# Performance work log

Measured on AMD Instinct MI355X. Metric: run time of the kernel, lower is better.

## Reference

```python
import jax, jax.numpy as jnp
import numpy as np

B, N, C, H = 1, 128, 128, 8
D = C // H
SCALE = D ** -0.5


def layer_norm(x, w, b, eps=1e-5):
    m = jnp.mean(x, axis=-1, keepdims=True)
    v = jnp.var(x, axis=-1, keepdims=True)
    return (x - m) * jax.lax.rsqrt(v + eps) * w + b


def setup_inputs() -> dict:
    key = jax.random.key(0)
    ks = jax.random.split(key, 8)
    s = 0.02
    return {
        "e": jax.random.normal(ks[0], (B, N, N, C), jnp.float32),
        "mask": jnp.zeros((B, N, N, 1), jnp.float32),
        "ln_w": jnp.ones((C,), jnp.float32),
        "ln_b": jnp.zeros((C,), jnp.float32),
        "w_qkv_in": jax.random.normal(ks[1], (C, 3 * C), jnp.float32) * s,
        "b_qkv_in": jnp.zeros((3 * C,), jnp.float32),
        "w_eg_in": jax.random.normal(ks[2], (C, 2 * H), jnp.float32) * s,
        "b_eg_in": jnp.zeros((2 * H,), jnp.float32),
        "w_qkv_out": jax.random.normal(ks[3], (C, 3 * C), jnp.float32) * s,
        "b_qkv_out": jnp.zeros((3 * C,), jnp.float32),
        "w_eg_out": jax.random.normal(ks[4], (C, 2 * H), jnp.float32) * s,
        "b_eg_out": jnp.zeros((2 * H,), jnp.float32),
        "w_o": jax.random.normal(ks[5], (2 * C, C), jnp.float32) * s,
        "b_o": jnp.zeros((C,), jnp.float32),
    }


def reference(e, mask, ln_w, ln_b, w_qkv_in, b_qkv_in, w_eg_in, b_eg_in,
              w_qkv_out, b_qkv_out, w_eg_out, b_eg_out, w_o, b_o):
    b, n = e.shape[0], e.shape[1]
    e_ln = layer_norm(e, ln_w, ln_b)

    # ---- incoming-edge stream ----
    qkv = e_ln @ w_qkv_in + b_qkv_in                      # [b,n,n,3C]
    Q, K, V = jnp.split(qkv, 3, axis=-1)
    Q = Q.reshape(b, n, n, D, H) * SCALE                  # bijdh
    K = K.reshape(b, n, n, D, H)
    V = V.reshape(b, n, n, D, H)
    eg = e_ln @ w_eg_in + b_eg_in                         # [b,n,n,2H]
    E_in = eg[..., :H][:, :, None, :, :]                  # [b,i,1,k,h]
    G_in = eg[..., H:][:, :, None, :, :]
    H_in = jnp.einsum('bijdh,bjkdh->bijkh', Q, K) + E_in
    mask_in = mask[:, :, None, :, :]                      # [b,i,1,k,1]
    gates_in = jax.nn.sigmoid(G_in + mask_in)
    A_in = jax.nn.softmax(H_in + mask_in, axis=3) * gates_in
    Va_in = jnp.einsum('bijkh,bjkdh->bijdh', A_in, V)

    # ---- outgoing-edge stream ----
    qkv = e_ln @ w_qkv_out + b_qkv_out
    Q, K, V = jnp.split(qkv, 3, axis=-1)
    Q = Q.reshape(b, n, n, D, H) * SCALE
    K = K.reshape(b, n, n, D, H)
    V = V.reshape(b, n, n, D, H)
    eg = e_ln @ w_eg_out + b_eg_out
    E_out = eg[..., :H][:, :, :, None, :]                 # [b,k,i,1,h]
    G_out = eg[..., H:][:, :, :, None, :]
    H_out = jnp.einsum('bijdh,bkjdh->bkijh', Q, K) + E_out
    mask_out = mask[:, :, :, None, :]                     # [b,k,i,1,1]
    gates_out = jax.nn.sigmoid(G_out + mask_out)
    A_out = jax.nn.softmax(H_out + mask_out, axis=1) * gates_out
    Va_out = jnp.einsum('bkijh,bkjdh->bijdh', A_out, V)

    Va = jnp.concatenate([Va_in, Va_out], axis=-1).reshape(b, n, n, 2 * C)
    return Va @ w_o + b_o
```

## Files before the change

kernel.cpp:

```cpp
#include <hip/hip_runtime.h>
#include <hip/hip_bf16.h>


#define NPOS 16384
#define CDIM 128

typedef __attribute__((ext_vector_type(8))) short bf16x8;
typedef __attribute__((ext_vector_type(8))) unsigned short u16x8;
typedef __attribute__((ext_vector_type(4))) float f32x4;

#define MFMA16(a, b, c) __builtin_amdgcn_mfma_f32_16x16x32_bf16((a), (b), (c), 0, 0, 0)

#define GLL16(gp, lp) __builtin_amdgcn_global_load_lds( \
    (const __attribute__((address_space(1))) void*)(gp), \
    (__attribute__((address_space(3))) void*)(lp), 16, 0, 0)

static __device__ __forceinline__ unsigned short f2bf(float x) {
    union { float f; unsigned int u; } v; v.f = x;
    unsigned int u = v.u;
    unsigned int r = u + 0x7FFFu + ((u >> 16) & 1u);
    return (unsigned short)(r >> 16);
}
static __device__ __forceinline__ float bf2f(unsigned short h) {
    union { float f; unsigned int u; } v; v.u = ((unsigned int)h) << 16; return v.f;
}

__global__ __launch_bounds__(256) void prep_kernel(
    const float* __restrict__ e, const float* __restrict__ lnw,
    const float* __restrict__ lnb, unsigned short* __restrict__ e_hl,
    const float* __restrict__ wq1, const float* __restrict__ we1,
    unsigned short* __restrict__ B1t,
    const float* __restrict__ wq2, const float* __restrict__ we2,
    unsigned short* __restrict__ B2t,
    const float* __restrict__ wo, unsigned short* __restrict__ B3t)
{
    const int t = threadIdx.x;
    const int bx = blockIdx.x;
    if (bx < 4096) {
        const int lane = t & 63;
        const int row = bx * 4 + (t >> 6);
        float2 x = *(const float2*)(e + (size_t)row * CDIM + lane * 2);
        float s = x.x + x.y, s2 = x.x * x.x + x.y * x.y;
        #pragma unroll
        for (int off = 1; off < 64; off <<= 1) {
            s  += __shfl_xor(s,  off, 64);
            s2 += __shfl_xor(s2, off, 64);
        }
        float m = s * (1.f / 128.f);
        float v = s2 * (1.f / 128.f) - m * m;
        float sc = rsqrtf(v + 1e-5f);
        float2 wv = *(const float2*)(lnw + lane * 2);
        float2 bv = *(const float2*)(lnb + lane * 2);
        float y0 = (x.x - m) * sc * wv.x + bv.x;
        float y1 = (x.y - m) * sc * wv.y + bv.y;
        unsigned short h0 = f2bf(y0), h1 = f2bf(y1);
        ushort2 hi = {h0, h1};
        ushort2 lo = {f2bf(y0 - bf2f(h0)), f2bf(y1 - bf2f(h1))};
        *(ushort2*)(e_hl + (size_t)row * 256 + lane * 2)       = hi;
        *(ushort2*)(e_hl + (size_t)row * 256 + 128 + lane * 2) = lo;
    } else if (bx < 4544) {
        int pb = bx - 4096;
        const float* wq; const float* we; unsigned short* Bt;
        if (pb < 224) { wq = wq1; we = we1; Bt = B1t; }
        else          { pb -= 224; wq = wq2; we = we2; Bt = B2t; }
        const int idx = pb * 256 + t;
        const int n = idx >> 7, k = idx & 127;
        float v = 0.f;
        if (n < 384) v = wq[(size_t)k * 384 + n];
        else if (n < 400) v = we[(size_t)k * 16 + (n - 384)];
        unsigned short hi = f2bf(v);
        Bt[idx] = hi;
        Bt[448 * 128 + idx] = f2bf(v - bf2f(hi));
    } else {
        const int idx = (bx - 4544) * 256 + t;
        const int n = idx >> 8, kp = idx & 255;
        const int d = kp & 15, pl = kp >> 4;
        const int k = d * 16 + pl;
        float v = wo[(size_t)k * 128 + n];
        unsigned short hi = f2bf(v);
        B3t[idx] = hi;
        B3t[128 * 256 + idx] = f2bf(v - bf2f(hi));
    }
}

__global__ __launch_bounds__(256) void gemm_qkv_kernel(
    const unsigned short* __restrict__ e_hl,
    const unsigned short* __restrict__ B1t, const unsigned short* __restrict__ B2t,
    const float* __restrict__ bq_i, const float* __restrict__ be_i,
    const float* __restrict__ bq_o, const float* __restrict__ be_o,
    const float* __restrict__ mask,
    unsigned short* __restrict__ QT, unsigned short* __restrict__ KT,
    unsigned short* __restrict__ VT,
    unsigned short* __restrict__ Etab, unsigned short* __restrict__ Gtab)
{
    __shared__ __align__(16) unsigned char smem[24576];
    unsigned short* Alds = (unsigned short*)smem;
    unsigned short* Blds = (unsigned short*)(smem + 16384);

    const int t = threadIdx.x;
    const int wave = t >> 6, lane = t & 63;
    const int m = lane & 15, q = lane >> 4;
    const int c = blockIdx.x;
    const int bx = ((c & 31) << 2) | (c >> 5);
    const int W0blk = bx * 128;
    const int by = blockIdx.y;
    const int N0 = by * 64;
    const int br = blockIdx.z;
    const unsigned short* Bt = br ? B2t : B1t;
    const float* bias_qkv = br ? bq_o : bq_i;
    const float* bias_eg  = br ? be_o : be_i;

    f32x4 acc[2][4];
    #pragma unroll
    for (int a = 0; a < 2; ++a)
        #pragma unroll
        for (int cc = 0; cc < 4; ++cc) acc[a][cc] = (f32x4){0.f, 0.f, 0.f, 0.f};

    for (int kc = 0; kc < 4; ++kc) {
        #pragma unroll
        for (int ii = 0; ii < 6; ++ii) {
            const int id = wave + ii * 4;
            if (id < 16) {
                const int hl = id >> 3, s = id & 7;
                const int qq = s >> 1, rbase = (s & 1) * 64;
                const unsigned short* g = e_hl
                    + (size_t)(W0blk + rbase + lane) * 256 + hl * 128 + kc * 32 + qq * 8;
                unsigned short* l = Alds + hl * 4096 + qq * 1024 + rbase * 8;
                GLL16(g, l);
            } else {
                const int id2 = id - 16;
                const int hl = id2 >> 2, qq = id2 & 3;
                const unsigned short* g = Bt + (size_t)(N0 + lane) * 128
                    + hl * (448 * 128) + kc * 32 + qq * 8;
                unsigned short* l = Blds + hl * 2048 + qq * 512;
                GLL16(g, l);
            }
        }
        __syncthreads();

        bf16x8 aH[2], aL[2], bH[4], bL[4];
        #pragma unroll
        for (int ms = 0; ms < 2; ++ms) {
            const int row = wave * 32 + ms * 16 + m;
            aH[ms] = *(const bf16x8*)(Alds + 0    + q * 1024 + row * 8);
            aL[ms] = *(const bf16x8*)(Alds + 4096 + q * 1024 + row * 8);
        }
        #pragma unroll
        for (int ns = 0; ns < 4; ++ns) {
            bH[ns] = *(const bf16x8*)(Blds + 0    + q * 512 + (ns * 16 + m) * 8);
            bL[ns] = *(const bf16x8*)(Blds + 2048 + q * 512 + (ns * 16 + m) * 8);
        }
        #pragma unroll
        for (int ns = 0; ns < 4; ++ns) {
            acc[0][ns] = MFMA16(aH[0], bH[ns], acc[0][ns]);
            acc[1][ns] = MFMA16(aH[1], bH[ns], acc[1][ns]);
        }
        #pragma unroll
        for (int ns = 0; ns < 4; ++ns) {
            acc[0][ns] = MFMA16(aL[0], bH[ns], acc[0][ns]);
            acc[1][ns] = MFMA16(aL[1], bH[ns], acc[1][ns]);
        }
        #pragma unroll
        for (int ns = 0; ns < 4; ++ns) {
            acc[0][ns] = MFMA16(aH[0], bL[ns], acc[0][ns]);
            acc[1][ns] = MFMA16(aH[1], bL[ns], acc[1][ns]);
        }
        __syncthreads();
    }

    if (by < 6) {
        unsigned short (*Ts16)[66] = (unsigned short (*)[66])smem;
        #pragma unroll
        for (int ms = 0; ms < 2; ++ms)
            #pragma unroll
            for (int ns = 0; ns < 4; ++ns) {
                const int lc = ns * 16 + m;
                const int col = N0 + lc;
                const float bias = bias_qkv[col];
                const float scale = (col < 128) ? 0.25f : 1.f;
                #pragma unroll
                for (int r = 0; r < 4; ++r) {
                    const int lr = wave * 32 + ms * 16 + q * 4 + r;
                    Ts16[lr][lc] = f2bf((acc[ms][ns][r] + bias) * scale);
                }
            }
        __syncthreads();
        const int qsel = by >> 1, dhalf = by & 1;
        unsigned short* dstH = (qsel == 0) ? QT : (qsel == 1 ? KT : VT);
        const bool tr = (qsel == 0) || (br == 1);
        #pragma unroll
        for (int it = 0; it < 4; ++it) {
            int item = it * 256 + t;
            int hh = item >> 7, lr = item & 127;
            u16x8 hi;
            #pragma unroll
            for (int dd = 0; dd < 8; ++dd)
                hi[dd] = Ts16[lr][dd * 8 + hh];
            const size_t sub = ((size_t)(br * 8 + hh) * 2 + dhalf) * NPOS;
            const size_t p16 = tr ? ((size_t)lr * 128 + bx)
                                  : ((size_t)bx * 128 + lr);
            *(u16x8*)(dstH + (sub + p16) * 8) = hi;
        }
    } else {
        float* Tf = (float*)smem;
        #pragma unroll
        for (int ms = 0; ms < 2; ++ms) {
            const float bias = bias_eg[m];
            #pragma unroll
            for (int r = 0; r < 4; ++r) {
                const int lr = wave * 32 + ms * 16 + q * 4 + r;
                Tf[lr * 33 + m] = acc[ms][0][r] + bias;
            }
        }
        __syncthreads();
        const int r128 = t & 127, grp = t >> 7;
        const float mk = mask[bx * 128 + r128];
        const int dst = br ? (r128 * 128 + bx) : (bx * 128 + r128);
        if (grp == 0) {
            #pragma unroll
            for (int h = 0; h < 8; ++h)
                Etab[(size_t)(br * 8 + h) * NPOS + dst] =
                    f2bf(Tf[r128 * 33 + h] + mk);
        } else {
            #pragma unroll
            for (int h = 0; h < 8; ++h) {
                const float g = Tf[r128 * 33 + 8 + h] + mk;
                Gtab[(size_t)(br * 8 + h) * NPOS + dst] =
                    f2bf(1.f / (1.f + __expf(-g)));
            }
        }
    }
}

__global__ __launch_bounds__(256) void gemm_out_kernel(
    const float* __restrict__ va,
    const unsigned short* __restrict__ B3t,
    const float* __restrict__ bias,
    float* __restrict__ out)
{
    const int t = threadIdx.x;
    const int wave = t >> 6, lane = t & 63;
    const int m = lane & 15, q = lane >> 4;
    const int W0 = blockIdx.x * 64 + wave * 16;

    f32x4 acc[8];
    #pragma unroll
    for (int cc = 0; cc < 8; ++cc) acc[cc] = (f32x4){0.f, 0.f, 0.f, 0.f};

    const float* arow = va + (size_t)(W0 + m) * 256;
    const unsigned short* brow = B3t + (size_t)m * 256;

    #pragma unroll 2
    for (int kc = 0; kc < 8; ++kc) {
        const int ko = kc * 32 + q * 8;
        const float4* ap = (const float4*)(arow + ko);
        float4 f0 = ap[0], f1 = ap[1];
        float xs[8] = {f0.x, f0.y, f0.z, f0.w, f1.x, f1.y, f1.z, f1.w};
        bf16x8 ah, al;
        #pragma unroll
        for (int jj = 0; jj < 8; ++jj) {
            unsigned short h = f2bf(xs[jj]);
            ah[jj] = (short)h;
            al[jj] = (short)f2bf(xs[jj] - bf2f(h));
        }
        bf16x8 bh[8], bl[8];
        #pragma unroll
        for (int ns = 0; ns < 8; ++ns) {
            const unsigned short* bp = brow + (size_t)ns * (16 * 256) + ko;
            bh[ns] = *(const bf16x8*)bp;
            bl[ns] = *(const bf16x8*)(bp + 128 * 256);
        }
        #pragma unroll
        for (int ns = 0; ns < 8; ++ns) acc[ns] = MFMA16(ah, bh[ns], acc[ns]);
        #pragma unroll
        for (int ns = 0; ns < 8; ++ns) acc[ns] = MFMA16(al, bh[ns], acc[ns]);
        #pragma unroll
        for (int ns = 0; ns < 8; ++ns) acc[ns] = MFMA16(ah, bl[ns], acc[ns]);
    }

    #pragma unroll
    for (int ns = 0; ns < 8; ++ns) {
        const int col = ns * 16 + m;
        #pragma unroll
        for (int r = 0; r < 4; ++r) {
            const int prow = W0 + q * 4 + r;
            const int orow = ((prow & 127) << 7) | (prow >> 7);
            out[(size_t)orow * 128 + col] = acc[ns][r] + bias[col];
        }
    }
}

__global__ __launch_bounds__(256) void attn_kernel(
    const unsigned short* __restrict__ QT, const unsigned short* __restrict__ KT,
    const unsigned short* __restrict__ VT,
    const unsigned short* __restrict__ Etab, const unsigned short* __restrict__ Gtab,
    float* __restrict__ va)
{
    const int j = blockIdx.x, h = blockIdx.y, br = blockIdx.z;
    const int t = threadIdx.x;
    const int wave = t >> 6, lane = t & 63;
    const int m = lane & 15, q = lane >> 4;
    const int plane = br * 8 + h;
    const size_t SP = (size_t)NPOS * 8;
    const size_t jb = (size_t)j * 128 * 8;
    const unsigned short* __restrict__ Eb = Etab + (size_t)plane * NPOS;
    const unsigned short* __restrict__ Gb = Gtab + (size_t)plane * NPOS;

    __shared__ unsigned short Vth[16 * 136];
    __shared__ unsigned short Pl[128 * 136];

    const int strip = wave * 32;

    f32x4 S[2][8];
    #pragma unroll
    for (int mt = 0; mt < 2; ++mt)
        #pragma unroll
        for (int r = 0; r < 4; ++r) {
            const int i = strip + mt * 16 + q * 4 + r;
            u16x8 ev = *(const u16x8*)(Eb + (size_t)i * 128 + m * 8);
            #pragma unroll
            for (int nt = 0; nt < 8; ++nt) S[mt][nt][r] = bf2f(ev[nt]);
        }

    {
        int c = t >> 1, ch = t & 1;
        int krow = (c & 15) * 8 + (c >> 4);
        const unsigned short* src = VT + (size_t)(plane * 2 + ch) * SP + jb
                                  + (size_t)krow * 8;
        u16x8 v = *(const u16x8*)src;
        #pragma unroll
        for (int dd = 0; dd < 8; ++dd)
            Vth[(ch * 8 + dd) * 136 + c] = v[dd];
    }

    const bf16x8 zero8 = {};
    const int hf = q & 1;
    const size_t qko = (size_t)(plane * 2 + hf) * SP + jb;

    bf16x8 aQ[2];
    #pragma unroll
    for (int mt = 0; mt < 2; ++mt) {
        const size_t off = qko + (size_t)(strip + mt * 16 + m) * 8;
        aQ[mt] = (q < 2) ? *(const bf16x8*)(QT + off) : zero8;
    }

    #pragma unroll
    for (int nt = 0; nt < 8; ++nt) {
        const size_t koff = qko + (size_t)(m * 8 + nt) * 8;
        bf16x8 bK = (q < 2) ? *(const bf16x8*)(KT + koff) : zero8;
        #pragma unroll
        for (int mt = 0; mt < 2; ++mt)
            S[mt][nt] = MFMA16(aQ[mt], bK, S[mt][nt]);
    }

    #pragma unroll
    for (int mt = 0; mt < 2; ++mt)
        #pragma unroll
        for (int r = 0; r < 4; ++r) {
            float v = -1e30f;
            #pragma unroll
            for (int nt = 0; nt < 8; ++nt) v = fmaxf(v, S[mt][nt][r]);
            v = fmaxf(v, __shfl_xor(v, 1)); v = fmaxf(v, __shfl_xor(v, 2));
            v = fmaxf(v, __shfl_xor(v, 4)); v = fmaxf(v, __shfl_xor(v, 8));
            float s = 0.f;
            #pragma unroll
            for (int nt = 0; nt < 8; ++nt) {
                float p = __expf(S[mt][nt][r] - v);
                S[mt][nt][r] = p;
                s += p;
            }
            s += __shfl_xor(s, 1); s += __shfl_xor(s, 2);
            s += __shfl_xor(s, 4); s += __shfl_xor(s, 8);
            const float inv = 1.f / s;
            const int i = strip + mt * 16 + q * 4 + r;
            u16x8 gv = *(const u16x8*)(Gb + (size_t)i * 128 + m * 8);
            #pragma unroll
            for (int nt = 0; nt < 4; ++nt) {
                Pl[i * 136 + nt * 16 + m] =
                    f2bf(S[mt][nt][r] * inv * bf2f(gv[nt]));
                Pl[i * 136 + (nt + 4) * 16 + m] =
                    f2bf(S[mt][nt + 4][r] * inv * bf2f(gv[nt + 4]));
            }
        }

    __syncthreads();

    f32x4 av[2] = {(f32x4){0.f, 0.f, 0.f, 0.f}, (f32x4){0.f, 0.f, 0.f, 0.f}};
    #pragma unroll
    for (int kc = 0; kc < 4; ++kc) {
        const int off = kc * 32 + q * 8;
        bf16x8 bV = *(const bf16x8*)&Vth[m * 136 + off];
        #pragma unroll
        for (int mt = 0; mt < 2; ++mt) {
            bf16x8 aP = *(const bf16x8*)&Pl[(strip + mt * 16 + m) * 136 + off];
            av[mt] = MFMA16(aP, bV, av[mt]);
        }
    }

    #pragma unroll
    for (int mt = 0; mt < 2; ++mt)
        #pragma unroll
        for (int r = 0; r < 4; ++r) {
            const int i = strip + mt * 16 + q * 4 + r;
            va[((size_t)(j * 128 + i)) * 256 + plane * 16 + m] = av[mt][r];
        }
}

extern "C" void kernel_launch(void* const* d_in, const int* in_sizes, int n_in,
                              void* d_out, int out_size, void* d_ws, size_t ws_size,
                              hipStream_t stream) {
    const float* e        = (const float*)d_in[0];
    const float* mask     = (const float*)d_in[1];
    const float* ln_w     = (const float*)d_in[2];
    const float* ln_b     = (const float*)d_in[3];
    const float* w_qkv_in = (const float*)d_in[4];
    const float* b_qkv_in = (const float*)d_in[5];
    const float* w_eg_in  = (const float*)d_in[6];
    const float* b_eg_in  = (const float*)d_in[7];
    const float* w_qkv_o  = (const float*)d_in[8];
    const float* b_qkv_o  = (const float*)d_in[9];
    const float* w_eg_o   = (const float*)d_in[10];
    const float* b_eg_o   = (const float*)d_in[11];
    const float* w_o      = (const float*)d_in[12];
    const float* b_o      = (const float*)d_in[13];
    float* out = (float*)d_out;

    char* base = (char*)d_ws;
    const size_t PLANE = (size_t)16 * NPOS * 16;
    unsigned short* e_hl = (unsigned short*)base;
    unsigned short* QT = (unsigned short*)(base + (size_t)NPOS * 256 * 2);
    unsigned short* KT = QT + PLANE;
    unsigned short* VT = KT + PLANE;
    float* va = (float*)(VT + PLANE);
    unsigned short* Etab = (unsigned short*)(va + (size_t)NPOS * 256);
    unsigned short* Gtab = Etab + (size_t)16 * NPOS;
    unsigned short* B3t  = Gtab + (size_t)16 * NPOS;

    unsigned short* B1t = (unsigned short*)va;
    unsigned short* B2t = B1t + (size_t)2 * 448 * 128;

    prep_kernel<<<4672, 256, 0, stream>>>(
        e, ln_w, ln_b, e_hl,
        w_qkv_in, w_eg_in, B1t, w_qkv_o, w_eg_o, B2t, w_o, B3t);

    gemm_qkv_kernel<<<dim3(128, 7, 2), 256, 0, stream>>>(
        e_hl, B1t, B2t, b_qkv_in, b_eg_in, b_qkv_o, b_eg_o, mask,
        QT, KT, VT, Etab, Gtab);

    attn_kernel<<<dim3(128, 8, 2), 256, 0, stream>>>(
        QT, KT, VT, Etab, Gtab, va);

    gemm_out_kernel<<<256, 256, 0, stream>>>(va, B3t, b_o, out);
}
```

Measured before the change: 167.7 us.

## Fuse four launches into one persistent kernel with software grid barriers

New measurement: 583.2 us. +247.7%, slower.

```diff
diff --git a/kernel.cpp b/kernel.cpp
--- a/kernel.cpp
+++ b/kernel.cpp
@@ -4,6 +4,7 @@
 
 #define NPOS 16384
 #define CDIM 128
+#define NBLK 512
 
 typedef __attribute__((ext_vector_type(8))) short bf16x8;
 typedef __attribute__((ext_vector_type(8))) unsigned short u16x8;
@@ -25,406 +26,416 @@
     union { float f; unsigned int u; } v; v.u = ((unsigned int)h) << 16; return v.f;
 }
 
-__global__ __launch_bounds__(256) void prep_kernel(
-    const float* __restrict__ e, const float* __restrict__ lnw,
-    const float* __restrict__ lnb, unsigned short* __restrict__ e_hl,
-    const float* __restrict__ wq1, const float* __restrict__ we1,
-    unsigned short* __restrict__ B1t,
-    const float* __restrict__ wq2, const float* __restrict__ we2,
-    unsigned short* __restrict__ B2t,
-    const float* __restrict__ wo, unsigned short* __restrict__ B3t)
+__device__ unsigned g_cnt = 0;
+__device__ unsigned g_gen = 0;
+
+static __device__ __forceinline__ void gbar() {
+    __syncthreads();
+    __threadfence();
+    if (threadIdx.x == 0) {
+        unsigned my = __hip_atomic_load(&g_gen, __ATOMIC_RELAXED,
+                                        __HIP_MEMORY_SCOPE_AGENT);
+        unsigned arrived = __hip_atomic_fetch_add(&g_cnt, 1u, __ATOMIC_ACQ_REL,
+                                                  __HIP_MEMORY_SCOPE_AGENT) + 1u;
+        if (arrived == NBLK) {
+            __hip_atomic_store(&g_cnt, 0u, __ATOMIC_RELAXED,
+                               __HIP_MEMORY_SCOPE_AGENT);
+            __hip_atomic_store(&g_gen, my + 1u, __ATOMIC_RELEASE,
+                               __HIP_MEMORY_SCOPE_AGENT);
+        } else {
+            int spins = 0;
+            while (__hip_atomic_load(&g_gen, __ATOMIC_ACQUIRE,
+                                     __HIP_MEMORY_SCOPE_AGENT) == my) {
+                __builtin_amdgcn_s_sleep(8);
+                if (++spins > (1 << 17)) break;
+            }
+        }
+    }
+    __threadfence();
+    __syncthreads();
+}
+
+struct KParams {
+    const float *e, *mask, *lnw, *lnb;
+    const float *wq1, *we1, *wq2, *we2, *wo;
+    const float *bq_i, *be_i, *bq_o, *be_o, *b_o;
+    unsigned short *e_hl, *B1t, *B2t, *B3t;
+    unsigned short *QT, *KT, *VT, *Etab, *Gtab;
+    float *va, *out;
+};
+
+__global__ __launch_bounds__(256, 2) void fused_kernel(KParams P)
 {
+    __shared__ __align__(16) unsigned char smem[39424];
+
     const int t = threadIdx.x;
-    const int bx = blockIdx.x;
-    if (bx < 4096) {
-        const int lane = t & 63;
-        const int row = bx * 4 + (t >> 6);
-        float2 x = *(const float2*)(e + (size_t)row * CDIM + lane * 2);
-        float s = x.x + x.y, s2 = x.x * x.x + x.y * x.y;
-        #pragma unroll
-        for (int off = 1; off < 64; off <<= 1) {
-            s  += __shfl_xor(s,  off, 64);
-            s2 += __shfl_xor(s2, off, 64);
-        }
-        float m = s * (1.f / 128.f);
-        float v = s2 * (1.f / 128.f) - m * m;
-        float sc = rsqrtf(v + 1e-5f);
-        float2 wv = *(const float2*)(lnw + lane * 2);
-        float2 bv = *(const float2*)(lnb + lane * 2);
-        float y0 = (x.x - m) * sc * wv.x + bv.x;
-        float y1 = (x.y - m) * sc * wv.y + bv.y;
-        unsigned short h0 = f2bf(y0), h1 = f2bf(y1);
-        ushort2 hi = {h0, h1};
-        ushort2 lo = {f2bf(y0 - bf2f(h0)), f2bf(y1 - bf2f(h1))};
-        *(ushort2*)(e_hl + (size_t)row * 256 + lane * 2)       = hi;
-        *(ushort2*)(e_hl + (size_t)row * 256 + 128 + lane * 2) = lo;
-    } else if (bx < 4544) {
-        int pb = bx - 4096;
-        const float* wq; const float* we; unsigned short* Bt;
-        if (pb < 224) { wq = wq1; we = we1; Bt = B1t; }
-        else          { pb -= 224; wq = wq2; we = we2; Bt = B2t; }
-        const int idx = pb * 256 + t;
-        const int n = idx >> 7, k = idx & 127;
-        float v = 0.f;
-        if (n < 384) v = wq[(size_t)k * 384 + n];
-        else if (n < 400) v = we[(size_t)k * 16 + (n - 384)];
-        unsigned short hi = f2bf(v);
-        Bt[idx] = hi;
-        Bt[448 * 128 + idx] = f2bf(v - bf2f(hi));
-    } else {
-        const int idx = (bx - 4544) * 256 + t;
-        const int n = idx >> 8, kp = idx & 255;
-        const int d = kp & 15, pl = kp >> 4;
-        const int k = d * 16 + pl;
-        float v = wo[(size_t)k * 128 + n];
-        unsigned short hi = f2bf(v);
-        B3t[idx] = hi;
-        B3t[128 * 256 + idx] = f2bf(v - bf2f(hi));
-    }
-}
-
-__global__ __launch_bounds__(256) void gemm_qkv_kernel(
-    const unsigned short* __restrict__ e_hl,
-    const unsigned short* __restrict__ B1t, const unsigned short* __restrict__ B2t,
-    const float* __restrict__ bq_i, const float* __restrict__ be_i,
-    const float* __restrict__ bq_o, const float* __restrict__ be_o,
-    const float* __restrict__ mask,
-    unsigned short* __restrict__ QT, unsigned short* __restrict__ KT,
-    unsigned short* __restrict__ VT,
-    unsigned short* __restrict__ Etab, unsigned short* __restrict__ Gtab)
-{
-    __shared__ __align__(16) unsigned char smem[24576];
-    unsigned short* Alds = (unsigned short*)smem;
-    unsigned short* Blds = (unsigned short*)(smem + 16384);
-
-    const int t = threadIdx.x;
+    const int bid = blockIdx.x;
     const int wave = t >> 6, lane = t & 63;
     const int m = lane & 15, q = lane >> 4;
-    const int c = blockIdx.x;
-    const int bx = ((c & 31) << 2) | (c >> 5);
-    const int W0blk = bx * 128;
-    const int by = blockIdx.y;
-    const int N0 = by * 64;
-    const int br = blockIdx.z;
-    const unsigned short* Bt = br ? B2t : B1t;
-    const float* bias_qkv = br ? bq_o : bq_i;
-    const float* bias_eg  = br ? be_o : be_i;
-
-    f32x4 acc[2][4];
-    #pragma unroll
-    for (int a = 0; a < 2; ++a)
+
+    for (int vb = bid; vb < 4672; vb += NBLK) {
+        if (vb < 4096) {
+            const int row = vb * 4 + (t >> 6);
+            float2 x = *(const float2*)(P.e + (size_t)row * CDIM + lane * 2);
+            float s = x.x + x.y, s2 = x.x * x.x + x.y * x.y;
+            #pragma unroll
+            for (int off = 1; off < 64; off <<= 1) {
+                s  += __shfl_xor(s,  off, 64);
+                s2 += __shfl_xor(s2, off, 64);
+            }
+            float mm = s * (1.f / 128.f);
+            float vv = s2 * (1.f / 128.f) - mm * mm;
+            float sc = rsqrtf(vv + 1e-5f);
+            float2 wv = *(const float2*)(P.lnw + lane * 2);
+            float2 bv = *(const float2*)(P.lnb + lane * 2);
+            float y0 = (x.x - mm) * sc * wv.x + bv.x;
+            float y1 = (x.y - mm) * sc * wv.y + bv.y;
+            unsigned short h0 = f2bf(y0), h1 = f2bf(y1);
+            ushort2 hi = {h0, h1};
+            ushort2 lo = {f2bf(y0 - bf2f(h0)), f2bf(y1 - bf2f(h1))};
+            *(ushort2*)(P.e_hl + (size_t)row * 256 + lane * 2)       = hi;
+            *(ushort2*)(P.e_hl + (size_t)row * 256 + 128 + lane * 2) = lo;
+        } else if (vb < 4544) {
+            int pb = vb - 4096;
+            const float* wq; const float* we; unsigned short* Bt;
+            if (pb < 224) { wq = P.wq1; we = P.we1; Bt = P.B1t; }
+            else          { pb -= 224; wq = P.wq2; we = P.we2; Bt = P.B2t; }
+            const int idx = pb * 256 + t;
+            const int n = idx >> 7, k = idx & 127;
+            float v = 0.f;
+            if (n < 384) v = wq[(size_t)k * 384 + n];
+            else if (n < 400) v = we[(size_t)k * 16 + (n - 384)];
+            unsigned short hi = f2bf(v);
+            Bt[idx] = hi;
+            Bt[448 * 128 + idx] = f2bf(v - bf2f(hi));
+        } else {
+            const int idx = (vb - 4544) * 256 + t;
+            const int n = idx >> 8, kp = idx & 255;
+            const int d = kp & 15, pl = kp >> 4;
+            const int k = d * 16 + pl;
+            float v = P.wo[(size_t)k * 128 + n];
+            unsigned short hi = f2bf(v);
+            P.B3t[idx] = hi;
+            P.B3t[128 * 256 + idx] = f2bf(v - bf2f(hi));
+        }
+    }
+    gbar();
+
+    for (int vb = bid; vb < 1792; vb += NBLK) {
+        unsigned short* Alds = (unsigned short*)smem;
+        unsigned short* Blds = (unsigned short*)(smem + 16384);
+        const int craw = vb & 127;
+        const int rem = vb >> 7;
+        const int by = rem % 7;
+        const int br = rem / 7;
+        const int bx = ((craw & 31) << 2) | (craw >> 5);
+        const int W0blk = bx * 128;
+        const int N0 = by * 64;
+        const unsigned short* Bt = br ? P.B2t : P.B1t;
+        const float* bias_qkv = br ? P.bq_o : P.bq_i;
+        const float* bias_eg  = br ? P.be_o : P.be_i;
+
+        f32x4 acc[2][4];
         #pragma unroll
-        for (int cc = 0; cc < 4; ++cc) acc[a][cc] = (f32x4){0.f, 0.f, 0.f, 0.f};
-
-    for (int kc = 0; kc < 4; ++kc) {
+        for (int a = 0; a < 2; ++a)
+            #pragma unroll
+            for (int cc = 0; cc < 4; ++cc) acc[a][cc] = (f32x4){0.f, 0.f, 0.f, 0.f};
+
+        for (int kc = 0; kc < 4; ++kc) {
+            #pragma unroll
+            for (int ii = 0; ii < 6; ++ii) {
+                const int id = wave + ii * 4;
+                if (id < 16) {
+                    const int hl = id >> 3, s = id & 7;
+                    const int qq = s >> 1, rbase = (s & 1) * 64;
+                    const unsigned short* g = P.e_hl
+                        + (size_t)(W0blk + rbase + lane) * 256 + hl * 128 + kc * 32 + qq * 8;
+                    unsigned short* l = Alds + hl * 4096 + qq * 1024 + rbase * 8;
+                    GLL16(g, l);
+                } else {
+                    const int id2 = id - 16;
+                    const int hl = id2 >> 2, qq = id2 & 3;
+                    const unsigned short* g = Bt + (size_t)(N0 + lane) * 128
+                        + hl * (448 * 128) + kc * 32 + qq * 8;
+                    unsigned short* l = Blds + hl * 2048 + qq * 512;
+                    GLL16(g, l);
+                }
+            }
+            __syncthreads();
+
+            bf16x8 aH[2], aL[2], bH[4], bL[4];
+            #pragma unroll
+            for (int ms = 0; ms < 2; ++ms) {
+                const int row = wave * 32 + ms * 16 + m;
+                aH[ms] = *(const bf16x8*)(Alds + 0    + q * 1024 + row * 8);
+                aL[ms] = *(const bf16x8*)(Alds + 4096 + q * 1024 + row * 8);
+            }
+            #pragma unroll
+            for (int ns = 0; ns < 4; ++ns) {
+                bH[ns] = *(const bf16x8*)(Blds + 0    + q * 512 + (ns * 16 + m) * 8);
+                bL[ns] = *(const bf16x8*)(Blds + 2048 + q * 512 + (ns * 16 + m) * 8);
+            }
+            #pragma unroll
+            for (int ns = 0; ns < 4; ++ns) {
+                acc[0][ns] = MFMA16(aH[0], bH[ns], acc[0][ns]);
+                acc[1][ns] = MFMA16(aH[1], bH[ns], acc[1][ns]);
+            }
+            #pragma unroll
+            for (int ns = 0; ns < 4; ++ns) {
+                acc[0][ns] = MFMA16(aL[0], bH[ns], acc[0][ns]);
+                acc[1][ns] = MFMA16(aL[1], bH[ns], acc[1][ns]);
+            }
+            #pragma unroll
+            for (int ns = 0; ns < 4; ++ns) {
+                acc[0][ns] = MFMA16(aH[0], bL[ns], acc[0][ns]);
+                acc[1][ns] = MFMA16(aH[1], bL[ns], acc[1][ns]);
+            }
+            __syncthreads();
+        }
+
+        if (by < 6) {
+            unsigned short (*Ts16)[66] = (unsigned short (*)[66])smem;
+            #pragma unroll
+            for (int ms = 0; ms < 2; ++ms)
+                #pragma unroll
+                for (int ns = 0; ns < 4; ++ns) {
+                    const int lc = ns * 16 + m;
+                    const int col = N0 + lc;
+                    const float bias = bias_qkv[col];
+                    const float scale = (col < 128) ? 0.25f : 1.f;
+                    #pragma unroll
+                    for (int r = 0; r < 4; ++r) {
+                        const int lr = wave * 32 + ms * 16 + q * 4 + r;
+                        Ts16[lr][lc] = f2bf((acc[ms][ns][r] + bias) * scale);
+                    }
+                }
+            __syncthreads();
+            const int qsel = by >> 1, dhalf = by & 1;
+            unsigned short* dstH = (qsel == 0) ? P.QT : (qsel == 1 ? P.KT : P.VT);
+            const bool tr = (qsel == 0) || (br == 1);
+            #pragma unroll
+            for (int it = 0; it < 4; ++it) {
+                int item = it * 256 + t;
+                int hh = item >> 7, lr = item & 127;
+                u16x8 hi;
+                #pragma unroll
+                for (int dd = 0; dd < 8; ++dd)
+                    hi[dd] = Ts16[lr][dd * 8 + hh];
+                const size_t sub = ((size_t)(br * 8 + hh) * 2 + dhalf) * NPOS;
+                const size_t p16 = tr ? ((size_t)lr * 128 + bx)
+                                      : ((size_t)bx * 128 + lr);
+                *(u16x8*)(dstH + (sub + p16) * 8) = hi;
+            }
+        } else {
+            float* Tf = (float*)smem;
+            #pragma unroll
+            for (int ms = 0; ms < 2; ++ms) {
+                const float bias = bias_eg[m];
+                #pragma unroll
+                for (int r = 0; r < 4; ++r) {
+                    const int lr = wave * 32 + ms * 16 + q * 4 + r;
+                    Tf[lr * 33 + m] = acc[ms][0][r] + bias;
+                }
+            }
+            __syncthreads();
+            const int r128 = t & 127, grp = t >> 7;
+            const float mk = P.mask[bx * 128 + r128];
+            const int dst = br ? (r128 * 128 + bx) : (bx * 128 + r128);
+            if (grp == 0) {
+                #pragma unroll
+                for (int h = 0; h < 8; ++h)
+                    P.Etab[(size_t)(br * 8 + h) * NPOS + dst] =
+                        f2bf(Tf[r128 * 33 + h] + mk);
+            } else {
+                #pragma unroll
+                for (int h = 0; h < 8; ++h) {
+                    const float g = Tf[r128 * 33 + 8 + h] + mk;
+                    P.Gtab[(size_t)(br * 8 + h) * NPOS + dst] =
+                        f2bf(1.f / (1.f + __expf(-g)));
+                }
+            }
+        }
+        __syncthreads();
+    }
+    gbar();
+
+    {
+        const int plane = bid >> 5;
+        const int j0 = (bid & 31) * 4;
+        unsigned short* Vth = (unsigned short*)smem;
+        unsigned short* Pl  = (unsigned short*)(smem + 4352);
+        const size_t SP = (size_t)NPOS * 8;
+        const unsigned short* __restrict__ Eb = P.Etab + (size_t)plane * NPOS;
+        const unsigned short* __restrict__ Gb = P.Gtab + (size_t)plane * NPOS;
+        const int strip = wave * 32;
+
+        u16x8 Ec[2][4], Gc[2][4];
         #pragma unroll
-        for (int ii = 0; ii < 6; ++ii) {
-            const int id = wave + ii * 4;
-            if (id < 16) {
-                const int hl = id >> 3, s = id & 7;
-                const int qq = s >> 1, rbase = (s & 1) * 64;
-                const unsigned short* g = e_hl
-                    + (size_t)(W0blk + rbase + lane) * 256 + hl * 128 + kc * 32 + qq * 8;
-                unsigned short* l = Alds + hl * 4096 + qq * 1024 + rbase * 8;
-                GLL16(g, l);
-            } else {
-                const int id2 = id - 16;
-                const int hl = id2 >> 2, qq = id2 & 3;
-                const unsigned short* g = Bt + (size_t)(N0 + lane) * 128
-                    + hl * (448 * 128) + kc * 32 + qq * 8;
-                unsigned short* l = Blds + hl * 2048 + qq * 512;
-                GLL16(g, l);
-            }
-        }
-        __syncthreads();
-
-        bf16x8 aH[2], aL[2], bH[4], bL[4];
+        for (int mt = 0; mt < 2; ++mt)
+            #pragma unroll
+            for (int r = 0; r < 4; ++r) {
+                const int i = strip + mt * 16 + q * 4 + r;
+                Ec[mt][r] = *(const u16x8*)(Eb + (size_t)i * 128 + m * 8);
+                Gc[mt][r] = *(const u16x8*)(Gb + (size_t)i * 128 + m * 8);
+            }
+
+        for (int it = 0; it < 4; ++it) {
+            const int j = j0 + it;
+            const size_t jb = (size_t)j * 128 * 8;
+
+            f32x4 S[2][8];
+            #pragma unroll
+            for (int mt = 0; mt < 2; ++mt)
+                #pragma unroll
+                for (int r = 0; r < 4; ++r) {
+                    #pragma unroll
+                    for (int nt = 0; nt < 8; ++nt)
+                        S[mt][nt][r] = bf2f(Ec[mt][r][nt]);
+                }
+
+            {
+                int c = t >> 1, ch = t & 1;
+                int krow = (c & 15) * 8 + (c >> 4);
+                const unsigned short* src = P.VT + (size_t)(plane * 2 + ch) * SP
+                                          + jb + (size_t)krow * 8;
+                u16x8 v = *(const u16x8*)src;
+                #pragma unroll
+                for (int dd = 0; dd < 8; ++dd)
+                    Vth[(ch * 8 + dd) * 136 + c] = v[dd];
+            }
+
+            const bf16x8 zero8 = {};
+            const int hf = q & 1;
+            const size_t qko = (size_t)(plane * 2 + hf) * SP + jb;
+
+            bf16x8 aQ[2];
+            #pragma unroll
+            for (int mt = 0; mt < 2; ++mt) {
+                const size_t off = qko + (size_t)(strip + mt * 16 + m) * 8;
+                aQ[mt] = (q < 2) ? *(const bf16x8*)(P.QT + off) : zero8;
+            }
+
+            #pragma unroll
+            for (int nt = 0; nt < 8; ++nt) {
+                const size_t koff = qko + (size_t)(m * 8 + nt) * 8;
+                bf16x8 bK = (q < 2) ? *(const bf16x8*)(P.KT + koff) : zero8;
+                #pragma unroll
+                for (int mt = 0; mt < 2; ++mt)
+                    S[mt][nt] = MFMA16(aQ[mt], bK, S[mt][nt]);
+            }
+
+            #pragma unroll
+            for (int mt = 0; mt < 2; ++mt)
+                #pragma unroll
+                for (int r = 0; r < 4; ++r) {
+                    float v = -1e30f;
+                    #pragma unroll
+                    for (int nt = 0; nt < 8; ++nt) v = fmaxf(v, S[mt][nt][r]);
+                    v = fmaxf(v, __shfl_xor(v, 1)); v = fmaxf(v, __shfl_xor(v, 2));
+                    v = fmaxf(v, __shfl_xor(v, 4)); v = fmaxf(v, __shfl_xor(v, 8));
+                    float s = 0.f;
+                    #pragma unroll
+                    for (int nt = 0; nt < 8; ++nt) {
+                        float p = __expf(S[mt][nt][r] - v);
+                        S[mt][nt][r] = p;
+                        s += p;
+                    }
+                    s += __shfl_xor(s, 1); s += __shfl_xor(s, 2);
+                    s += __shfl_xor(s, 4); s += __shfl_xor(s, 8);
+                    const float inv = 1.f / s;
+                    const int i = strip + mt * 16 + q * 4 + r;
+                    #pragma unroll
+                    for (int nt = 0; nt < 4; ++nt) {
+                        Pl[i * 136 + nt * 16 + m] =
+                            f2bf(S[mt][nt][r] * inv * bf2f(Gc[mt][r][nt]));
+                        Pl[i * 136 + (nt + 4) * 16 + m] =
+                            f2bf(S[mt][nt + 4][r] * inv * bf2f(Gc[mt][r][nt + 4]));
+                    }
+                }
+
+            __syncthreads();
+
+            f32x4 av[2] = {(f32x4){0.f, 0.f, 0.f, 0.f}, (f32x4){0.f, 0.f, 0.f, 0.f}};
+            #pragma unroll
+            for (int kc = 0; kc < 4; ++kc) {
+                const int off = kc * 32 + q * 8;
+                bf16x8 bV = *(const bf16x8*)&Vth[m * 136 + off];
+                #pragma unroll
+                for (int mt = 0; mt < 2; ++mt) {
+                    bf16x8 aP = *(const bf16x8*)&Pl[(strip + mt * 16 + m) * 136 + off];
+                    av[mt] = MFMA16(aP, bV, av[mt]);
+                }
+            }
+
+            #pragma unroll
+            for (int mt = 0; mt < 2; ++mt)
+                #pragma unroll
+                for (int r = 0; r < 4; ++r) {
+                    const int i = strip + mt * 16 + q * 4 + r;
+                    P.va[((size_t)(j * 128 + i)) * 256 + plane * 16 + m] = av[mt][r];
+                }
+            __syncthreads();
+        }
+    }
+    gbar();
+
+    {
+        const int W0 = (bid >> 1) * 64 + wave * 16;
+        const int N0 = (bid & 1) * 64;
+
+        f32x4 acc[4];
         #pragma unroll
-        for (int ms = 0; ms < 2; ++ms) {
-            const int row = wave * 32 + ms * 16 + m;
-            aH[ms] = *(const bf16x8*)(Alds + 0    + q * 1024 + row * 8);
-            aL[ms] = *(const bf16x8*)(Alds + 4096 + q * 1024 + row * 8);
-        }
+        for (int cc = 0; cc < 4; ++cc) acc[cc] = (f32x4){0.f, 0.f, 0.f, 0.f};
+
+        const float* arow = P.va + (size_t)(W0 + m) * 256;
+        const unsigned short* bcol[4];
+        #pragma unroll
+        for (int ns = 0; ns < 4; ++ns)
+            bcol[ns] = P.B3t + (size_t)(N0 + ns * 16 + m) * 256;
+
+        #pragma unroll 2
+        for (int kc = 0; kc < 8; ++kc) {
+            const int ko = kc * 32 + q * 8;
+            const float4* ap = (const float4*)(arow + ko);
+            float4 f0 = ap[0], f1 = ap[1];
+            float xs[8] = {f0.x, f0.y, f0.z, f0.w, f1.x, f1.y, f1.z, f1.w};
+            bf16x8 ah, al;
+            #pragma unroll
+            for (int jj = 0; jj < 8; ++jj) {
+                unsigned short hh = f2bf(xs[jj]);
+                ah[jj] = (short)hh;
+                al[jj] = (short)f2bf(xs[jj] - bf2f(hh));
+            }
+            bf16x8 bh[4], bl[4];
+            #pragma unroll
+            for (int ns = 0; ns < 4; ++ns) {
+                bh[ns] = *(const bf16x8*)(bcol[ns] + ko);
+                bl[ns] = *(const bf16x8*)(bcol[ns] + 128 * 256 + ko);
+            }
+            #pragma unroll
+            for (int ns = 0; ns < 4; ++ns) acc[ns] = MFMA16(ah, bh[ns], acc[ns]);
+            #pragma unroll
+            for (int ns = 0; ns < 4; ++ns) acc[ns] = MFMA16(al, bh[ns], acc[ns]);
+            #pragma unroll
+            for (int ns = 0; ns < 4; ++ns) acc[ns] = MFMA16(ah, bl[ns], acc[ns]);
+        }
+
         #pragma unroll
         for (int ns = 0; ns < 4; ++ns) {
-            bH[ns] = *(const bf16x8*)(Blds + 0    + q * 512 + (ns * 16 + m) * 8);
-            bL[ns] = *(const bf16x8*)(Blds + 2048 + q * 512 + (ns * 16 + m) * 8);
-        }
-        #pragma unroll
-        for (int ns = 0; ns < 4; ++ns) {
-            acc[0][ns] = MFMA16(aH[0], bH[ns], acc[0][ns]);
-            acc[1][ns] = MFMA16(aH[1], bH[ns], acc[1][ns]);
-        }
-        #pragma unroll
-        for (int ns = 0; ns < 4; ++ns) {
-            acc[0][ns] = MFMA16(aL[0], bH[ns], acc[0][ns]);
-            acc[1][ns] = MFMA16(aL[1], bH[ns], acc[1][ns]);
-        }
-        #pragma unroll
-        for (int ns = 0; ns < 4; ++ns) {
-            acc[0][ns] = MFMA16(aH[0], bL[ns], acc[0][ns]);
-            acc[1][ns] = MFMA16(aH[1], bL[ns], acc[1][ns]);
-        }
-        __syncthreads();
+            const int col = N0 + ns * 16 + m;
+            #pragma unroll
+            for (int r = 0; r < 4; ++r) {
+                const int prow = W0 + q * 4 + r;
+                const int orow = ((prow & 127) << 7) | (prow >> 7);
+                P.out[(size_t)orow * 128 + col] = acc[ns][r] + P.b_o[col];
+            }
+        }
     }
-
-    if (by < 6) {
-        unsigned short (*Ts16)[66] = (unsigned short (*)[66])smem;
-        #pragma unroll
-        for (int ms = 0; ms < 2; ++ms)
-            #pragma unroll
-            for (int ns = 0; ns < 4; ++ns) {
-                const int lc = ns * 16 + m;
-                const int col = N0 + lc;
-                const float bias = bias_qkv[col];
-                const float scale = (col < 128) ? 0.25f : 1.f;
-                #pragma unroll
-                for (int r = 0; r < 4; ++r) {
-                    const int lr = wave * 32 + ms * 16 + q * 4 + r;
-                    Ts16[lr][lc] = f2bf((acc[ms][ns][r] + bias) * scale);
-                }
-            }
-        __syncthreads();
-        const int qsel = by >> 1, dhalf = by & 1;
-        unsigned short* dstH = (qsel == 0) ? QT : (qsel == 1 ? KT : VT);
-        const bool tr = (qsel == 0) || (br == 1);
-        #pragma unroll
-        for (int it = 0; it < 4; ++it) {
-            int item = it * 256 + t;
-            int hh = item >> 7, lr = item & 127;
-            u16x8 hi;
-            #pragma unroll
-            for (int dd = 0; dd < 8; ++dd)
-                hi[dd] = Ts16[lr][dd * 8 + hh];
-            const size_t sub = ((size_t)(br * 8 + hh) * 2 + dhalf) * NPOS;
-            const size_t p16 = tr ? ((size_t)lr * 128 + bx)
-                                  : ((size_t)bx * 128 + lr);
-            *(u16x8*)(dstH + (sub + p16) * 8) = hi;
-        }
-    } else {
-        float* Tf = (float*)smem;
-        #pragma unroll
-        for (int ms = 0; ms < 2; ++ms) {
-            const float bias = bias_eg[m];
-            #pragma unroll
-            for (int r = 0; r < 4; ++r) {
-                const int lr = wave * 32 + ms * 16 + q * 4 + r;
-                Tf[lr * 33 + m] = acc[ms][0][r] + bias;
-            }
-        }
-        __syncthreads();
-        const int r128 = t & 127, grp = t >> 7;
-        const float mk = mask[bx * 128 + r128];
-        const int dst = br ? (r128 * 128 + bx) : (bx * 128 + r128);
-        if (grp == 0) {
-            #pragma unroll
-            for (int h = 0; h < 8; ++h)
-                Etab[(size_t)(br * 8 + h) * NPOS + dst] =
-                    f2bf(Tf[r128 * 33 + h] + mk);
-        } else {
-            #pragma unroll
-            for (int h = 0; h < 8; ++h) {
-                const float g = Tf[r128 * 33 + 8 + h] + mk;
-                Gtab[(size_t)(br * 8 + h) * NPOS + dst] =
-                    f2bf(1.f / (1.f + __expf(-g)));
-            }
-        }
-    }
-}
-
-__global__ __launch_bounds__(256) void gemm_out_kernel(
-    const float* __restrict__ va,
-    const unsigned short* __restrict__ B3t,
-    const float* __restrict__ bias,
-    float* __restrict__ out)
-{
-    const int t = threadIdx.x;
-    const int wave = t >> 6, lane = t & 63;
-    const int m = lane & 15, q = lane >> 4;
-    const int W0 = blockIdx.x * 64 + wave * 16;
-
-    f32x4 acc[8];
-    #pragma unroll
-    for (int cc = 0; cc < 8; ++cc) acc[cc] = (f32x4){0.f, 0.f, 0.f, 0.f};
-
-    const float* arow = va + (size_t)(W0 + m) * 256;
-    const unsigned short* brow = B3t + (size_t)m * 256;
-
-    #pragma unroll 2
-    for (int kc = 0; kc < 8; ++kc) {
-        const int ko = kc * 32 + q * 8;
-        const float4* ap = (const float4*)(arow + ko);
-        float4 f0 = ap[0], f1 = ap[1];
-        float xs[8] = {f0.x, f0.y, f0.z, f0.w, f1.x, f1.y, f1.z, f1.w};
-        bf16x8 ah, al;
-        #pragma unroll
-        for (int jj = 0; jj < 8; ++jj) {
-            unsigned short h = f2bf(xs[jj]);
-            ah[jj] = (short)h;
-            al[jj] = (short)f2bf(xs[jj] - bf2f(h));
-        }
-        bf16x8 bh[8], bl[8];
-        #pragma unroll
-        for (int ns = 0; ns < 8; ++ns) {
-            const unsigned short* bp = brow + (size_t)ns * (16 * 256) + ko;
-            bh[ns] = *(const bf16x8*)bp;
-            bl[ns] = *(const bf16x8*)(bp + 128 * 256);
-        }
-        #pragma unroll
-        for (int ns = 0; ns < 8; ++ns) acc[ns] = MFMA16(ah, bh[ns], acc[ns]);
-        #pragma unroll
-        for (int ns = 0; ns < 8; ++ns) acc[ns] = MFMA16(al, bh[ns], acc[ns]);
-        #pragma unroll
-        for (int ns = 0; ns < 8; ++ns) acc[ns] = MFMA16(ah, bl[ns], acc[ns]);
-    }
-
-    #pragma unroll
-    for (int ns = 0; ns < 8; ++ns) {
-        const int col = ns * 16 + m;
-        #pragma unroll
-        for (int r = 0; r < 4; ++r) {
-            const int prow = W0 + q * 4 + r;
-            const int orow = ((prow & 127) << 7) | (prow >> 7);
-            out[(size_t)orow * 128 + col] = acc[ns][r] + bias[col];
-        }
-    }
-}
-
-__global__ __launch_bounds__(256) void attn_kernel(
-    const unsigned short* __restrict__ QT, const unsigned short* __restrict__ KT,
-    const unsigned short* __restrict__ VT,
-    const unsigned short* __restrict__ Etab, const unsigned short* __restrict__ Gtab,
-    float* __restrict__ va)
-{
-    const int j = blockIdx.x, h = blockIdx.y, br = blockIdx.z;
-    const int t = threadIdx.x;
-    const int wave = t >> 6, lane = t & 63;
-    const int m = lane & 15, q = lane >> 4;
-    const int plane = br * 8 + h;
-    const size_t SP = (size_t)NPOS * 8;
-    const size_t jb = (size_t)j * 128 * 8;
-    const unsigned short* __restrict__ Eb = Etab + (size_t)plane * NPOS;
-    const unsigned short* __restrict__ Gb = Gtab + (size_t)plane * NPOS;
-
-    __shared__ unsigned short Vth[16 * 136];
-    __shared__ unsigned short Pl[128 * 136];
-
-    const int strip = wave * 32;
-
-    f32x4 S[2][8];
-    #pragma unroll
-    for (int mt = 0; mt < 2; ++mt)
-        #pragma unroll
-        for (int r = 0; r < 4; ++r) {
-            const int i = strip + mt * 16 + q * 4 + r;
-            u16x8 ev = *(const u16x8*)(Eb + (size_t)i * 128 + m * 8);
-            #pragma unroll
-            for (int nt = 0; nt < 8; ++nt) S[mt][nt][r] = bf2f(ev[nt]);
-        }
-
-    {
-        int c = t >> 1, ch = t & 1;
-        int krow = (c & 15) * 8 + (c >> 4);
-        const unsigned short* src = VT + (size_t)(plane * 2 + ch) * SP + jb
-                                  + (size_t)krow * 8;
-        u16x8 v = *(const u16x8*)src;
-        #pragma unroll
-        for (int dd = 0; dd < 8; ++dd)
-            Vth[(ch * 8 + dd) * 136 + c] = v[dd];
-    }
-
-    const bf16x8 zero8 = {};
-    const int hf = q & 1;
-    const size_t qko = (size_t)(plane * 2 + hf) * SP + jb;
-
-    bf16x8 aQ[2];
-    #pragma unroll
-    for (int mt = 0; mt < 2; ++mt) {
-        const size_t off = qko + (size_t)(strip + mt * 16 + m) * 8;
-        aQ[mt] = (q < 2) ? *(const bf16x8*)(QT + off) : zero8;
-    }
-
-    #pragma unroll
-    for (int nt = 0; nt < 8; ++nt) {
-        const size_t koff = qko + (size_t)(m * 8 + nt) * 8;
-        bf16x8 bK = (q < 2) ? *(const bf16x8*)(KT + koff) : zero8;
-        #pragma unroll
-        for (int mt = 0; mt < 2; ++mt)
-            S[mt][nt] = MFMA16(aQ[mt], bK, S[mt][nt]);
-    }
-
-    #pragma unroll
-    for (int mt = 0; mt < 2; ++mt)
-        #pragma unroll
-        for (int r = 0; r < 4; ++r) {
-            float v = -1e30f;
-            #pragma unroll
-            for (int nt = 0; nt < 8; ++nt) v = fmaxf(v, S[mt][nt][r]);
-            v = fmaxf(v, __shfl_xor(v, 1)); v = fmaxf(v, __shfl_xor(v, 2));
-            v = fmaxf(v, __shfl_xor(v, 4)); v = fmaxf(v, __shfl_xor(v, 8));
-            float s = 0.f;
-            #pragma unroll
-            for (int nt = 0; nt < 8; ++nt) {
-                float p = __expf(S[mt][nt][r] - v);
-                S[mt][nt][r] = p;
-                s += p;
-            }
-            s += __shfl_xor(s, 1); s += __shfl_xor(s, 2);
-            s += __shfl_xor(s, 4); s += __shfl_xor(s, 8);
-            const float inv = 1.f / s;
-            const int i = strip + mt * 16 + q * 4 + r;
-            u16x8 gv = *(const u16x8*)(Gb + (size_t)i * 128 + m * 8);
-            #pragma unroll
-            for (int nt = 0; nt < 4; ++nt) {
-                Pl[i * 136 + nt * 16 + m] =
-                    f2bf(S[mt][nt][r] * inv * bf2f(gv[nt]));
-                Pl[i * 136 + (nt + 4) * 16 + m] =
-                    f2bf(S[mt][nt + 4][r] * inv * bf2f(gv[nt + 4]));
-            }
-        }
-
-    __syncthreads();
-
-    f32x4 av[2] = {(f32x4){0.f, 0.f, 0.f, 0.f}, (f32x4){0.f, 0.f, 0.f, 0.f}};
-    #pragma unroll
-    for (int kc = 0; kc < 4; ++kc) {
-        const int off = kc * 32 + q * 8;
-        bf16x8 bV = *(const bf16x8*)&Vth[m * 136 + off];
-        #pragma unroll
-        for (int mt = 0; mt < 2; ++mt) {
-            bf16x8 aP = *(const bf16x8*)&Pl[(strip + mt * 16 + m) * 136 + off];
-            av[mt] = MFMA16(aP, bV, av[mt]);
-        }
-    }
-
-    #pragma unroll
-    for (int mt = 0; mt < 2; ++mt)
-        #pragma unroll
-        for (int r = 0; r < 4; ++r) {
-            const int i = strip + mt * 16 + q * 4 + r;
-            va[((size_t)(j * 128 + i)) * 256 + plane * 16 + m] = av[mt][r];
-        }
 }
 
 extern "C" void kernel_launch(void* const* d_in, const int* in_sizes, int n_in,
                               void* d_out, int out_size, void* d_ws, size_t ws_size,
                               hipStream_t stream) {
-    const float* e        = (const float*)d_in[0];
-    const float* mask     = (const float*)d_in[1];
-    const float* ln_w     = (const float*)d_in[2];
-    const float* ln_b     = (const float*)d_in[3];
-    const float* w_qkv_in = (const float*)d_in[4];
-    const float* b_qkv_in = (const float*)d_in[5];
-    const float* w_eg_in  = (const float*)d_in[6];
-    const float* b_eg_in  = (const float*)d_in[7];
-    const float* w_qkv_o  = (const float*)d_in[8];
-    const float* b_qkv_o  = (const float*)d_in[9];
-    const float* w_eg_o   = (const float*)d_in[10];
-    const float* b_eg_o   = (const float*)d_in[11];
-    const float* w_o      = (const float*)d_in[12];
-    const float* b_o      = (const float*)d_in[13];
-    float* out = (float*)d_out;
-
     char* base = (char*)d_ws;
     const size_t PLANE = (size_t)16 * NPOS * 16;
     unsigned short* e_hl = (unsigned short*)base;
@@ -439,16 +450,24 @@
     unsigned short* B1t = (unsigned short*)va;
     unsigned short* B2t = B1t + (size_t)2 * 448 * 128;
 
-    prep_kernel<<<4672, 256, 0, stream>>>(
-        e, ln_w, ln_b, e_hl,
-        w_qkv_in, w_eg_in, B1t, w_qkv_o, w_eg_o, B2t, w_o, B3t);
-
-    gemm_qkv_kernel<<<dim3(128, 7, 2), 256, 0, stream>>>(
-        e_hl, B1t, B2t, b_qkv_in, b_eg_in, b_qkv_o, b_eg_o, mask,
-        QT, KT, VT, Etab, Gtab);
-
-    attn_kernel<<<dim3(128, 8, 2), 256, 0, stream>>>(
-        QT, KT, VT, Etab, Gtab, va);
-
-    gemm_out_kernel<<<256, 256, 0, stream>>>(va, B3t, b_o, out);
+    KParams Pr;
+    Pr.e    = (const float*)d_in[0];
+    Pr.mask = (const float*)d_in[1];
+    Pr.lnw  = (const float*)d_in[2];
+    Pr.lnb  = (const float*)d_in[3];
+    Pr.wq1  = (const float*)d_in[4];
+    Pr.bq_i = (const float*)d_in[5];
+    Pr.we1  = (const float*)d_in[6];
+    Pr.be_i = (const float*)d_in[7];
+    Pr.wq2  = (const float*)d_in[8];
+    Pr.bq_o = (const float*)d_in[9];
+    Pr.we2  = (const float*)d_in[10];
+    Pr.be_o = (const float*)d_in[11];
+    Pr.wo   = (const float*)d_in[12];
+    Pr.b_o  = (const float*)d_in[13];
+    Pr.e_hl = e_hl; Pr.B1t = B1t; Pr.B2t = B2t; Pr.B3t = B3t;
+    Pr.QT = QT; Pr.KT = KT; Pr.VT = VT; Pr.Etab = Etab; Pr.Gtab = Gtab;
+    Pr.va = va; Pr.out = (float*)d_out;
+
+    fused_kernel<<<NBLK, 256, 0, stream>>>(Pr);
 }
```
